# Kernel optimization log

Measured on AMD Instinct MI355X. Metric: run time of the kernel, lower is better.

## Reference

```python
import jax, jax.numpy as jnp
import numpy as np

B, I, J = 2, 2048, 2048
DIM = 1024
H = 16
DH = 64
INNER = H * DH
EPS = 1e-5


def _layernorm(x, g, b):
    mu = jnp.mean(x, axis=-1, keepdims=True)
    var = jnp.var(x, axis=-1, keepdims=True)
    return (x - mu) * jax.lax.rsqrt(var + EPS) * g + b


def setup_inputs() -> dict:
    key = jax.random.key(0)
    ks = jax.random.split(key, 12)
    s_in = 1.0 / np.sqrt(DIM)
    s_inner = 1.0 / np.sqrt(INNER)
    s_h = 1.0 / np.sqrt(H)
    return {
        "x": jax.random.normal(ks[0], (B, I, DIM), jnp.float32),
        "context": jax.random.normal(ks[1], (B, J, DIM), jnp.float32),
        "ln_g": jnp.ones((DIM,), jnp.float32),
        "ln_b": jnp.zeros((DIM,), jnp.float32),
        "ctx_ln_g": jnp.ones((DIM,), jnp.float32),
        "ctx_ln_b": jnp.zeros((DIM,), jnp.float32),
        "W_qk": jax.random.normal(ks[2], (DIM, INNER), jnp.float32) * s_in,
        "W_ctx_qk": jax.random.normal(ks[3], (DIM, INNER), jnp.float32) * s_in,
        "W_v": jax.random.normal(ks[4], (DIM, INNER), jnp.float32) * s_in,
        "W_ctx_v": jax.random.normal(ks[5], (DIM, INNER), jnp.float32) * s_in,
        "W_out": jax.random.normal(ks[6], (INNER, DIM), jnp.float32) * s_inner,
        "b_out": jnp.zeros((DIM,), jnp.float32),
        "W_ctx_out": jax.random.normal(ks[7], (INNER, DIM), jnp.float32) * s_inner,
        "b_ctx_out": jnp.zeros((DIM,), jnp.float32),
        "th_w": jax.random.normal(ks[8], (H, H), jnp.float32) * s_h,
        "ctx_th_w": jax.random.normal(ks[9], (H, H), jnp.float32) * s_h,
    }


def reference(x, context, ln_g, ln_b, ctx_ln_g, ctx_ln_b, W_qk, W_ctx_qk,
              W_v, W_ctx_v, W_out, b_out, W_ctx_out, b_ctx_out, th_w, ctx_th_w):
    b, i, j = x.shape[0], x.shape[1], context.shape[1]
    scale = DH ** -0.5
    xn = _layernorm(x, ln_g, ln_b)
    cn = _layernorm(context, ctx_ln_g, ctx_ln_b)

    def split_heads(t):  # [b, n, h*d] -> [b, h, n, d]
        return t.reshape(t.shape[0], t.shape[1], H, DH).transpose(0, 2, 1, 3)

    qk = split_heads(xn @ W_qk)            # [b, h, i, d]
    ctx_qk = split_heads(cn @ W_ctx_qk)    # [b, h, j, d]
    v = split_heads(xn @ W_v)              # [b, h, i, d]
    ctx_v = split_heads(cn @ W_ctx_v)      # [b, h, j, d]

    sim = jnp.einsum('bhid,bhjd->bhij', qk, ctx_qk) * scale  # shared sim matrix
    attn = jax.nn.softmax(sim, axis=-1)       # softmax over j
    ctx_attn = jax.nn.softmax(sim, axis=-2)   # softmax over i

    # talking heads: 1x1 conv over head dim
    attn = jnp.einsum('gh,bhij->bgij', th_w, attn)
    ctx_attn = jnp.einsum('gh,bhij->bgij', ctx_th_w, ctx_attn)

    out = jnp.einsum('bhij,bhjd->bhid', attn, ctx_v)       # [b, h, i, d]
    ctx_out = jnp.einsum('bhij,bhid->bhjd', ctx_attn, v)   # [b, h, j, d]

    def merge_heads(t):  # [b, h, n, d] -> [b, n, h*d]
        return t.transpose(0, 2, 1, 3).reshape(t.shape[0], t.shape[2], INNER)

    out = merge_heads(out) @ W_out + b_out
    ctx_out = merge_heads(ctx_out) @ W_ctx_out + b_ctx_out
    return out, ctx_out
```

## Files before the change

kernel.cpp:

```cpp
#include <hip/hip_runtime.h>
#include <hip/hip_bf16.h>
#include <cstdint>

#define DIM_   1024
#define H_     16
#define DH_    64
#define INNER_ 1024
#define B_     2
#define I_     2048
#define J_     2048
#define SCALE_ 0.125f

using bf16x8 = __attribute__((ext_vector_type(8))) short;
using f32x4  = __attribute__((ext_vector_type(4))) float;

__device__ __forceinline__ unsigned short f2bf(float f) {
  unsigned int u = __float_as_uint(f);
  u = (u + 0x7FFFu + ((u >> 16) & 1u)) >> 16;
  return (unsigned short)u;
}
__device__ __forceinline__ float bf2f(unsigned short h) {
  return __uint_as_float(((unsigned int)h) << 16);
}

__global__ __launch_bounds__(256) void ln_cast_kernel(
    const float* __restrict__ in, const float* __restrict__ g,
    const float* __restrict__ bb, unsigned short* __restrict__ out) {
  int row = blockIdx.x;
  int t = threadIdx.x;
  const float4* rp = (const float4*)(in + (size_t)row * DIM_);
  float4 v = rp[t];
  float s  = v.x + v.y + v.z + v.w;
  float ss = v.x * v.x + v.y * v.y + v.z * v.z + v.w * v.w;
  for (int o = 1; o < 64; o <<= 1) {
    s  += __shfl_xor(s, o, 64);
    ss += __shfl_xor(ss, o, 64);
  }
  __shared__ float ls[4], lss[4];
  int wave = t >> 6, lane = t & 63;
  if (lane == 0) { ls[wave] = s; lss[wave] = ss; }
  __syncthreads();
  s  = ls[0] + ls[1] + ls[2] + ls[3];
  ss = lss[0] + lss[1] + lss[2] + lss[3];
  float mu  = s * (1.0f / DIM_);
  float var = ss * (1.0f / DIM_) - mu * mu;
  float rstd = rsqrtf(var + 1e-5f);
  float4 gv = ((const float4*)g)[t];
  float4 bv = ((const float4*)bb)[t];
  ushort4 o4;
  o4.x = f2bf((v.x - mu) * rstd * gv.x + bv.x);
  o4.y = f2bf((v.y - mu) * rstd * gv.y + bv.y);
  o4.z = f2bf((v.z - mu) * rstd * gv.z + bv.z);
  o4.w = f2bf((v.w - mu) * rstd * gv.w + bv.w);
  ((ushort4*)(out + (size_t)row * DIM_))[t] = o4;
}

__global__ __launch_bounds__(256) void transpose_cast_f32(
    const float* __restrict__ in, unsigned short* __restrict__ out, int R, int C) {
  __shared__ float tile[32][33];
  int z = blockIdx.z;
  const float* ip = in + (size_t)z * R * C;
  unsigned short* op = out + (size_t)z * R * C;
  int c0 = blockIdx.x * 32, r0 = blockIdx.y * 32;
  int tx = threadIdx.x, ty = threadIdx.y;
  for (int k = 0; k < 4; k++)
    tile[ty * 4 + k][tx] = ip[(size_t)(r0 + ty * 4 + k) * C + c0 + tx];
  __syncthreads();
  for (int k = 0; k < 4; k++)
    op[(size_t)(c0 + ty * 4 + k) * R + r0 + tx] = f2bf(tile[tx][ty * 4 + k]);
}

__global__ __launch_bounds__(256) void transpose_bf16(
    const unsigned short* __restrict__ in, unsigned short* __restrict__ out, int R, int C) {
  __shared__ unsigned short tile[32][33];
  int z = blockIdx.z;
  const unsigned short* ip = in + (size_t)z * R * C;
  unsigned short* op = out + (size_t)z * R * C;
  int c0 = blockIdx.x * 32, r0 = blockIdx.y * 32;
  int tx = threadIdx.x, ty = threadIdx.y;
  for (int k = 0; k < 4; k++)
    tile[ty * 4 + k][tx] = ip[(size_t)(r0 + ty * 4 + k) * C + c0 + tx];
  __syncthreads();
  for (int k = 0; k < 4; k++)
    op[(size_t)(c0 + ty * 4 + k) * R + r0 + tx] = tile[tx][ty * 4 + k];
}

#define LDP 40
__global__ __launch_bounds__(256) void gemm_bt(
    const unsigned short* __restrict__ A, const unsigned short* __restrict__ Bt,
    const float* __restrict__ bias, void* __restrict__ Cout,
    int M, int N, int K, int c_f32) {
  __shared__ unsigned short As[128 * LDP];
  __shared__ unsigned short Bs[128 * LDP];
  int t = threadIdx.x;
  int lane = t & 63, wave = t >> 6;
  int m0 = blockIdx.y * 128, n0 = blockIdx.x * 128;
  int wm = (wave >> 1) * 64, wn = (wave & 1) * 64;
  int l15 = lane & 15, lk = lane >> 4;
  int lrow = t >> 2, lc8 = (t & 3) * 8;
  f32x4 acc[4][4] = {};

  for (int k0 = 0; k0 < K; k0 += 32) {
    *(bf16x8*)&As[lrow * LDP + lc8]        = *(const bf16x8*)&A[(size_t)(m0 + lrow) * K + k0 + lc8];
    *(bf16x8*)&As[(lrow + 64) * LDP + lc8] = *(const bf16x8*)&A[(size_t)(m0 + lrow + 64) * K + k0 + lc8];
    *(bf16x8*)&Bs[lrow * LDP + lc8]        = *(const bf16x8*)&Bt[(size_t)(n0 + lrow) * K + k0 + lc8];
    *(bf16x8*)&Bs[(lrow + 64) * LDP + lc8] = *(const bf16x8*)&Bt[(size_t)(n0 + lrow + 64) * K + k0 + lc8];
    __syncthreads();
    bf16x8 af[4], bfr[4];
#pragma unroll
    for (int mi = 0; mi < 4; mi++) af[mi]  = *(const bf16x8*)&As[(wm + mi * 16 + l15) * LDP + lk * 8];
#pragma unroll
    for (int ni = 0; ni < 4; ni++) bfr[ni] = *(const bf16x8*)&Bs[(wn + ni * 16 + l15) * LDP + lk * 8];
#pragma unroll
    for (int mi = 0; mi < 4; mi++)
#pragma unroll
      for (int ni = 0; ni < 4; ni++)
        acc[mi][ni] = __builtin_amdgcn_mfma_f32_16x16x32_bf16(af[mi], bfr[ni], acc[mi][ni], 0, 0, 0);
    __syncthreads();
  }
#pragma unroll
  for (int mi = 0; mi < 4; mi++)
#pragma unroll
    for (int ni = 0; ni < 4; ni++) {
      int col = n0 + wn + ni * 16 + l15;
      float bsv = bias ? bias[col] : 0.0f;
#pragma unroll
      for (int r = 0; r < 4; r++) {
        int row = m0 + wm + mi * 16 + lk * 4 + r;
        float val = acc[mi][ni][r] + bsv;
        if (c_f32) ((float*)Cout)[(size_t)row * N + col] = val;
        else ((unsigned short*)Cout)[(size_t)row * N + col] = f2bf(val);
      }
    }
}

__global__ __launch_bounds__(256) void stats_kernel(
    const unsigned short* __restrict__ Q, const unsigned short* __restrict__ Kc,
    float* __restrict__ rsum, int NQ, int NK) {
  int b = blockIdx.z, h = blockIdx.y, i0 = blockIdx.x * 32;
  int t = threadIdx.x, lane = t & 63, wave = t >> 6;
  int l15 = lane & 15, lk = lane >> 4;
  const size_t qbase = ((size_t)b * NQ + i0) * INNER_ + h * DH_;
  bf16x8 af[2][2];
#pragma unroll
  for (int mi = 0; mi < 2; mi++)
#pragma unroll
    for (int ks = 0; ks < 2; ks++)
      af[mi][ks] = *(const bf16x8*)&Q[qbase + (size_t)(mi * 16 + l15) * INNER_ + ks * 32 + lk * 8];
  float racc[2][4] = {};
  for (int j0 = wave * 16; j0 < NK; j0 += 64) {
    const size_t kbase = ((size_t)b * NK + j0 + l15) * INNER_ + h * DH_ + lk * 8;
    bf16x8 b0 = *(const bf16x8*)&Kc[kbase];
    bf16x8 b1 = *(const bf16x8*)&Kc[kbase + 32];
#pragma unroll
    for (int mi = 0; mi < 2; mi++) {
      f32x4 acc = {};
      acc = __builtin_amdgcn_mfma_f32_16x16x32_bf16(af[mi][0], b0, acc, 0, 0, 0);
      acc = __builtin_amdgcn_mfma_f32_16x16x32_bf16(af[mi][1], b1, acc, 0, 0, 0);
#pragma unroll
      for (int r = 0; r < 4; r++) racc[mi][r] += __expf(acc[r] * SCALE_);
    }
  }
#pragma unroll
  for (int o = 1; o < 16; o <<= 1)
#pragma unroll
    for (int mi = 0; mi < 2; mi++)
#pragma unroll
      for (int r = 0; r < 4; r++) racc[mi][r] += __shfl_xor(racc[mi][r], o, 64);
  __shared__ float part[4][32];
  if (l15 == 0)
#pragma unroll
    for (int mi = 0; mi < 2; mi++)
#pragma unroll
      for (int r = 0; r < 4; r++) part[wave][mi * 16 + lk * 4 + r] = racc[mi][r];
  __syncthreads();
  if (t < 32)
    rsum[((size_t)b * H_ + h) * NQ + i0 + t] = part[0][t] + part[1][t] + part[2][t] + part[3][t];
}

#define MSROW 40
#define MSG   (32 * MSROW + 8)
__global__ __launch_bounds__(256, 2) void fused_attn_kernel(
    const unsigned short* __restrict__ Q, const unsigned short* __restrict__ Kc,
    const unsigned short* __restrict__ Vt, const float* __restrict__ rsum,
    const float* __restrict__ thw,
    float* __restrict__ p0, float* __restrict__ p1,
    float* __restrict__ p2, float* __restrict__ p3,
    int NQ, int NK, int CHUNK) {
  __shared__ unsigned short Pb[4 * 256 * 16];
  __shared__ unsigned short Ms[16 * MSG];
  __shared__ float rinvS[512];
  int n = blockIdx.x;
  int combo = n & 7;
  int b = combo >> 2, jc = combo & 3;
  int i0 = (n >> 3) * 32;
  float* __restrict__ Op = (jc == 0) ? p0 : (jc == 1) ? p1 : (jc == 2) ? p2 : p3;
  int t = threadIdx.x, lane = t & 63, wave = t >> 6;
  int l15 = lane & 15, lk = lane >> 4;

  rinvS[t]       = 1.0f / rsum[((size_t)b * H_ + (t >> 5)) * NQ + i0 + (t & 31)];
  rinvS[t + 256] = 1.0f / rsum[((size_t)b * H_ + ((t + 256) >> 5)) * NQ + i0 + (t & 31)];

  bf16x8 tfrag;
  {
    int part = lk >> 1, hb = (lk & 1) * 8;
#pragma unroll
    for (int e = 0; e < 8; e++) {
      float a = thw[l15 * H_ + hb + e];
      unsigned short hi = f2bf(a);
      tfrag[e] = (short)(part == 0 ? hi : f2bf(a - bf2f(hi)));
    }
  }
  __syncthreads();

  bf16x8 qpre[4][2][2];
#pragma unroll
  for (int hh = 0; hh < 4; hh++)
#pragma unroll
    for (int is = 0; is < 2; is++)
#pragma unroll
      for (int kk = 0; kk < 2; kk++)
        qpre[hh][is][kk] = *(const bf16x8*)&Q[((size_t)b * NQ + i0 + is * 16 + l15) * INNER_
                                              + (wave * 4 + hh) * 64 + kk * 32 + lk * 8];

  f32x4 acc[32] = {};
  const int jbeg = jc * CHUNK;

  for (int js = 0; js < CHUNK; js += 32) {
    int j0 = jbeg + js;
    const unsigned short* Kb0 = Kc + ((size_t)b * NK + j0 + l15) * INNER_;
    const unsigned short* Kb1 = Kb0 + (size_t)16 * INNER_;
    unsigned int stage[2][2][4][2];
#pragma unroll
    for (int hh = 0; hh < 4; hh++) {
      int h = wave * 4 + hh;
      bf16x8 kb00 = *(const bf16x8*)&Kb0[h * 64 + lk * 8];
      bf16x8 kb01 = *(const bf16x8*)&Kb0[h * 64 + 32 + lk * 8];
      bf16x8 kb10 = *(const bf16x8*)&Kb1[h * 64 + lk * 8];
      bf16x8 kb11 = *(const bf16x8*)&Kb1[h * 64 + 32 + lk * 8];
#pragma unroll
      for (int is = 0; is < 2; is++) {
        f32x4 s0 = {}, s1 = {};
        s0 = __builtin_amdgcn_mfma_f32_16x16x32_bf16(qpre[hh][is][0], kb00, s0, 0, 0, 0);
        s0 = __builtin_amdgcn_mfma_f32_16x16x32_bf16(qpre[hh][is][1], kb01, s0, 0, 0, 0);
        s1 = __builtin_amdgcn_mfma_f32_16x16x32_bf16(qpre[hh][is][0], kb10, s1, 0, 0, 0);
        s1 = __builtin_amdgcn_mfma_f32_16x16x32_bf16(qpre[hh][is][1], kb11, s1, 0, 0, 0);
        f32x4 ri = *(const f32x4*)&rinvS[h * 32 + is * 16 + lk * 4];
#pragma unroll
        for (int r = 0; r < 4; r++) {
          unsigned int b0 = f2bf(__expf(s0[r] * SCALE_) * ri[r]);
          unsigned int b1 = f2bf(__expf(s1[r] * SCALE_) * ri[r]);
          if (hh & 1) { stage[is][0][r][hh >> 1] |= b0 << 16; stage[is][1][r][hh >> 1] |= b1 << 16; }
          else        { stage[is][0][r][hh >> 1]  = b0;       stage[is][1][r][hh >> 1]  = b1; }
        }
      }
    }
#pragma unroll
    for (int is = 0; is < 2; is++)
#pragma unroll
      for (int jp = 0; jp < 2; jp++)
#pragma unroll
        for (int r = 0; r < 4; r++) {
          int row = (lk * 4 + r) * 16 + l15;
          int col = (wave * 4) ^ ((row & 1) << 3);
          uint2 u = { stage[is][jp][r][0], stage[is][jp][r][1] };
          *(uint2*)&Pb[(is + jp * 2) * 256 * 16 + row * 16 + col] = u;
        }
    __syncthreads();
    {
      int isub = wave & 1, jstrip = wave >> 1;
      const unsigned short* pr = &Pb[(isub + jstrip * 2) * 256 * 16];
#pragma unroll
      for (int p = 0; p < 16; p++) {
        int row = p * 16 + l15;
        int col = ((lk & 1) << 3) ^ ((row & 1) << 3);
        bf16x8 af = *(const bf16x8*)&pr[row * 16 + col];
        f32x4 m = {};
        m = __builtin_amdgcn_mfma_f32_16x16x32_bf16(af, tfrag, m, 0, 0, 0);
        ushort4 o;
        o.x = f2bf(m[0]); o.y = f2bf(m[1]); o.z = f2bf(m[2]); o.w = f2bf(m[3]);
        *(ushort4*)&Ms[l15 * MSG + (isub * 16 + p) * MSROW + jstrip * 16 + lk * 4] = o;
      }
    }
    __syncthreads();
#pragma unroll
    for (int gi = 0; gi < 4; gi++) {
      int g = wave * 4 + gi;
      bf16x8 ma0 = *(const bf16x8*)&Ms[g * MSG + l15 * MSROW + lk * 8];
      bf16x8 ma1 = *(const bf16x8*)&Ms[g * MSG + (16 + l15) * MSROW + lk * 8];
#pragma unroll
      for (int nt = 0; nt < 4; nt++) {
        const size_t vb = ((size_t)b * INNER_ + g * 64 + nt * 16 + l15) * NK + j0 + lk * 8;
        bf16x8 v0 = *(const bf16x8*)&Vt[vb];
        acc[gi * 8 + nt]     = __builtin_amdgcn_mfma_f32_16x16x32_bf16(ma0, v0, acc[gi * 8 + nt], 0, 0, 0);
        acc[gi * 8 + 4 + nt] = __builtin_amdgcn_mfma_f32_16x16x32_bf16(ma1, v0, acc[gi * 8 + 4 + nt], 0, 0, 0);
      }
    }
  }
#pragma unroll
  for (int gi = 0; gi < 4; gi++)
#pragma unroll
    for (int is = 0; is < 2; is++)
#pragma unroll
      for (int nt = 0; nt < 4; nt++) {
        int col = (wave * 4 + gi) * 64 + nt * 16 + l15;
#pragma unroll
        for (int r = 0; r < 4; r++)
          Op[((size_t)b * NQ + i0 + is * 16 + lk * 4 + r) * INNER_ + col] = acc[gi * 8 + is * 4 + nt][r];
      }
}

__global__ __launch_bounds__(256) void reduce_cast_kernel(
    const float* __restrict__ p0, const float* __restrict__ p1,
    const float* __restrict__ p2, const float* __restrict__ p3,
    unsigned short* __restrict__ out, int n4) {
  int idx = blockIdx.x * 256 + threadIdx.x;
  if (idx >= n4) return;
  float4 v = ((const float4*)p0)[idx];
  float4 w = ((const float4*)p1)[idx];
  float4 a = ((const float4*)p2)[idx];
  float4 c = ((const float4*)p3)[idx];
  v.x += w.x + a.x + c.x; v.y += w.y + a.y + c.y;
  v.z += w.z + a.z + c.z; v.w += w.w + a.w + c.w;
  ushort4 o;
  o.x = f2bf(v.x); o.y = f2bf(v.y); o.z = f2bf(v.z); o.w = f2bf(v.w);
  ((ushort4*)out)[idx] = o;
}

extern "C" void kernel_launch(void* const* d_in, const int* in_sizes, int n_in,
                              void* d_out, int out_size, void* d_ws, size_t ws_size,
                              hipStream_t stream) {
  const float* x      = (const float*)d_in[0];
  const float* ctx    = (const float*)d_in[1];
  const float* ln_g   = (const float*)d_in[2];
  const float* ln_b   = (const float*)d_in[3];
  const float* cln_g  = (const float*)d_in[4];
  const float* cln_b  = (const float*)d_in[5];
  const float* W_qk   = (const float*)d_in[6];
  const float* W_cqk  = (const float*)d_in[7];
  const float* W_v    = (const float*)d_in[8];
  const float* W_cv   = (const float*)d_in[9];
  const float* W_out  = (const float*)d_in[10];
  const float* b_out  = (const float*)d_in[11];
  const float* W_cout = (const float*)d_in[12];
  const float* b_cout = (const float*)d_in[13];
  const float* th_w   = (const float*)d_in[14];
  const float* cth_w  = (const float*)d_in[15];

  char* w = (char*)d_ws;
  const size_t SZ_ROW = (size_t)B_ * I_ * DIM_ * 2;
  const size_t SZ_W   = (size_t)DIM_ * INNER_ * 2;
  unsigned short* xn    = (unsigned short*)w; w += SZ_ROW;
  unsigned short* cn    = (unsigned short*)w; w += SZ_ROW;
  unsigned short* Wqkt  = (unsigned short*)w; w += SZ_W;
  unsigned short* Wcqkt = (unsigned short*)w; w += SZ_W;
  unsigned short* Wvt   = (unsigned short*)w; w += SZ_W;
  unsigned short* Wcvt  = (unsigned short*)w; w += SZ_W;
  unsigned short* Woutt = (unsigned short*)w; w += SZ_W;
  unsigned short* Wcoutt= (unsigned short*)w; w += SZ_W;
  unsigned short* qk    = (unsigned short*)w; w += SZ_ROW;
  unsigned short* ck    = (unsigned short*)w; w += SZ_ROW;
  unsigned short* vv    = (unsigned short*)w; w += SZ_ROW;
  unsigned short* cv    = (unsigned short*)w; w += SZ_ROW;
  unsigned short* vT    = (unsigned short*)w; w += SZ_ROW;
  unsigned short* cvT   = (unsigned short*)w; w += SZ_ROW;
  float* rsum = (float*)w; w += (size_t)B_ * H_ * I_ * 4;
  float* csum = (float*)w; w += (size_t)B_ * H_ * J_ * 4;
  unsigned short* Oh1 = (unsigned short*)w; w += SZ_ROW;
  unsigned short* Oh2 = (unsigned short*)w; w += SZ_ROW;

  const size_t PART = (size_t)B_ * I_ * INNER_ * 4;
  float* p0 = (float*)xn;
  float* p1 = (float*)vv;
  float* p2 = (float*)w;
  float* p3 = (float*)(w + PART);

  dim3 tb(32, 8);
  ln_cast_kernel<<<B_ * I_, 256, 0, stream>>>(x, ln_g, ln_b, xn);
  ln_cast_kernel<<<B_ * J_, 256, 0, stream>>>(ctx, cln_g, cln_b, cn);

  transpose_cast_f32<<<dim3(32, 32, 1), tb, 0, stream>>>(W_qk,   Wqkt,  DIM_, INNER_);
  transpose_cast_f32<<<dim3(32, 32, 1), tb, 0, stream>>>(W_cqk,  Wcqkt, DIM_, INNER_);
  transpose_cast_f32<<<dim3(32, 32, 1), tb, 0, stream>>>(W_v,    Wvt,   DIM_, INNER_);
  transpose_cast_f32<<<dim3(32, 32, 1), tb, 0, stream>>>(W_cv,   Wcvt,  DIM_, INNER_);
  transpose_cast_f32<<<dim3(32, 32, 1), tb, 0, stream>>>(W_out,  Woutt, INNER_, DIM_);
  transpose_cast_f32<<<dim3(32, 32, 1), tb, 0, stream>>>(W_cout, Wcoutt,INNER_, DIM_);

  gemm_bt<<<dim3(INNER_ / 128, (B_ * I_) / 128), 256, 0, stream>>>(xn, Wqkt,  nullptr, qk, B_ * I_, INNER_, DIM_, 0);
  gemm_bt<<<dim3(INNER_ / 128, (B_ * J_) / 128), 256, 0, stream>>>(cn, Wcqkt, nullptr, ck, B_ * J_, INNER_, DIM_, 0);
  gemm_bt<<<dim3(INNER_ / 128, (B_ * I_) / 128), 256, 0, stream>>>(xn, Wvt,   nullptr, vv, B_ * I_, INNER_, DIM_, 0);
  gemm_bt<<<dim3(INNER_ / 128, (B_ * J_) / 128), 256, 0, stream>>>(cn, Wcvt,  nullptr, cv, B_ * J_, INNER_, DIM_, 0);

  transpose_bf16<<<dim3(INNER_ / 32, I_ / 32, B_), tb, 0, stream>>>(vv, vT, I_, INNER_);
  transpose_bf16<<<dim3(INNER_ / 32, J_ / 32, B_), tb, 0, stream>>>(cv, cvT, J_, INNER_);

  stats_kernel<<<dim3(I_ / 32, H_, B_), 256, 0, stream>>>(qk, ck, rsum, I_, J_);
  stats_kernel<<<dim3(J_ / 32, H_, B_), 256, 0, stream>>>(ck, qk, csum, J_, I_);

  const int n4 = (B_ * I_ * INNER_) / 4;
  fused_attn_kernel<<<(I_ / 32) * 4 * B_, 256, 0, stream>>>(
      qk, ck, cvT, rsum, th_w, p0, p1, p2, p3, I_, J_, J_ / 4);
  reduce_cast_kernel<<<n4 / 256, 256, 0, stream>>>(p0, p1, p2, p3, Oh1, n4);
  fused_attn_kernel<<<(J_ / 32) * 4 * B_, 256, 0, stream>>>(
      ck, qk, vT, csum, cth_w, p0, p1, p2, p3, J_, I_, I_ / 4);
  reduce_cast_kernel<<<n4 / 256, 256, 0, stream>>>(p0, p1, p2, p3, Oh2, n4);

  gemm_bt<<<dim3(DIM_ / 128, (B_ * I_) / 128), 256, 0, stream>>>(Oh1, Woutt, b_out, (float*)d_out, B_ * I_, DIM_, INNER_, 1);
  gemm_bt<<<dim3(DIM_ / 128, (B_ * J_) / 128), 256, 0, stream>>>(Oh2, Wcoutt, b_cout, ((float*)d_out) + (size_t)B_ * I_ * DIM_, B_ * J_, DIM_, INNER_, 1);
}
```

Measured before the change: 924.7 us.

## Batch projection GEMMs and stats launches, raise MFMA wave priority in attention

Concatenates the transposed QK and V weights so one batched GEMM launch (grid z over x/context) produces all four projections, and merges the two output projections into one launch. The stats kernel now handles both softmax directions in one launch and 64 rows per block, so each loaded K fragment is reused across more rows. The fused attention kernel wraps its MFMA sequences in s_setprio to favour issuing matrix ops across waves. The goal is fewer launches and tail effects, more reuse in stats, and better MFMA issue, at the cost of more registers in the stats kernel.

Result: faster. 806.4 us (-12.8%).

```diff
diff --git a/kernel.cpp b/kernel.cpp
--- a/kernel.cpp
+++ b/kernel.cpp
@@ -86,12 +86,19 @@
 }
 
 #define LDP 40
-__global__ __launch_bounds__(256) void gemm_bt(
-    const unsigned short* __restrict__ A, const unsigned short* __restrict__ Bt,
-    const float* __restrict__ bias, void* __restrict__ Cout,
-    int M, int N, int K, int c_f32) {
+__global__ __launch_bounds__(256) void gemm_qkv(
+    const unsigned short* __restrict__ A0, const unsigned short* __restrict__ A1,
+    const unsigned short* __restrict__ Bt0, const unsigned short* __restrict__ Bt1,
+    unsigned short* __restrict__ qkO0, unsigned short* __restrict__ vO0,
+    unsigned short* __restrict__ qkO1, unsigned short* __restrict__ vO1,
+    int M, int K) {
   __shared__ unsigned short As[128 * LDP];
   __shared__ unsigned short Bs[128 * LDP];
+  int z = blockIdx.z;
+  const unsigned short* A  = z ? A1 : A0;
+  const unsigned short* Bt = z ? Bt1 : Bt0;
+  unsigned short* qkO = z ? qkO1 : qkO0;
+  unsigned short* vO  = z ? vO1 : vO0;
   int t = threadIdx.x;
   int lane = t & 63, wave = t >> 6;
   int m0 = blockIdx.y * 128, n0 = blockIdx.x * 128;
@@ -118,42 +125,99 @@
         acc[mi][ni] = __builtin_amdgcn_mfma_f32_16x16x32_bf16(af[mi], bfr[ni], acc[mi][ni], 0, 0, 0);
     __syncthreads();
   }
+  unsigned short* dst = (n0 < 1024) ? qkO : vO;
+  int nbase = n0 & 1023;
+#pragma unroll
+  for (int mi = 0; mi < 4; mi++)
+#pragma unroll
+    for (int ni = 0; ni < 4; ni++) {
+      int col = nbase + wn + ni * 16 + l15;
+#pragma unroll
+      for (int r = 0; r < 4; r++) {
+        int row = m0 + wm + mi * 16 + lk * 4 + r;
+        dst[(size_t)row * INNER_ + col] = f2bf(acc[mi][ni][r]);
+      }
+    }
+}
+
+__global__ __launch_bounds__(256) void gemm_out(
+    const unsigned short* __restrict__ A0, const unsigned short* __restrict__ A1,
+    const unsigned short* __restrict__ Bt0, const unsigned short* __restrict__ Bt1,
+    const float* __restrict__ bias0, const float* __restrict__ bias1,
+    float* __restrict__ C0, float* __restrict__ C1,
+    int M, int N, int K) {
+  __shared__ unsigned short As[128 * LDP];
+  __shared__ unsigned short Bs[128 * LDP];
+  int z = blockIdx.z;
+  const unsigned short* A  = z ? A1 : A0;
+  const unsigned short* Bt = z ? Bt1 : Bt0;
+  const float* bias = z ? bias1 : bias0;
+  float* Cout = z ? C1 : C0;
+  int t = threadIdx.x;
+  int lane = t & 63, wave = t >> 6;
+  int m0 = blockIdx.y * 128, n0 = blockIdx.x * 128;
+  int wm = (wave >> 1) * 64, wn = (wave & 1) * 64;
+  int l15 = lane & 15, lk = lane >> 4;
+  int lrow = t >> 2, lc8 = (t & 3) * 8;
+  f32x4 acc[4][4] = {};
+
+  for (int k0 = 0; k0 < K; k0 += 32) {
+    *(bf16x8*)&As[lrow * LDP + lc8]        = *(const bf16x8*)&A[(size_t)(m0 + lrow) * K + k0 + lc8];
+    *(bf16x8*)&As[(lrow + 64) * LDP + lc8] = *(const bf16x8*)&A[(size_t)(m0 + lrow + 64) * K + k0 + lc8];
+    *(bf16x8*)&Bs[lrow * LDP + lc8]        = *(const bf16x8*)&Bt[(size_t)(n0 + lrow) * K + k0 + lc8];
+    *(bf16x8*)&Bs[(lrow + 64) * LDP + lc8] = *(const bf16x8*)&Bt[(size_t)(n0 + lrow + 64) * K + k0 + lc8];
+    __syncthreads();
+    bf16x8 af[4], bfr[4];
+#pragma unroll
+    for (int mi = 0; mi < 4; mi++) af[mi]  = *(const bf16x8*)&As[(wm + mi * 16 + l15) * LDP + lk * 8];
+#pragma unroll
+    for (int ni = 0; ni < 4; ni++) bfr[ni] = *(const bf16x8*)&Bs[(wn + ni * 16 + l15) * LDP + lk * 8];
+#pragma unroll
+    for (int mi = 0; mi < 4; mi++)
+#pragma unroll
+      for (int ni = 0; ni < 4; ni++)
+        acc[mi][ni] = __builtin_amdgcn_mfma_f32_16x16x32_bf16(af[mi], bfr[ni], acc[mi][ni], 0, 0, 0);
+    __syncthreads();
+  }
 #pragma unroll
   for (int mi = 0; mi < 4; mi++)
 #pragma unroll
     for (int ni = 0; ni < 4; ni++) {
       int col = n0 + wn + ni * 16 + l15;
-      float bsv = bias ? bias[col] : 0.0f;
+      float bsv = bias[col];
 #pragma unroll
       for (int r = 0; r < 4; r++) {
         int row = m0 + wm + mi * 16 + lk * 4 + r;
-        float val = acc[mi][ni][r] + bsv;
-        if (c_f32) ((float*)Cout)[(size_t)row * N + col] = val;
-        else ((unsigned short*)Cout)[(size_t)row * N + col] = f2bf(val);
+        Cout[(size_t)row * N + col] = acc[mi][ni][r] + bsv;
       }
     }
 }
 
 __global__ __launch_bounds__(256) void stats_kernel(
-    const unsigned short* __restrict__ Q, const unsigned short* __restrict__ Kc,
-    float* __restrict__ rsum, int NQ, int NK) {
-  int b = blockIdx.z, h = blockIdx.y, i0 = blockIdx.x * 32;
+    const unsigned short* __restrict__ qk, const unsigned short* __restrict__ ck,
+    float* __restrict__ rsum, float* __restrict__ csum, int NQ, int NK) {
+  int zz = blockIdx.z;
+  int b = zz & 1, dir = zz >> 1;
+  const unsigned short* Q  = dir ? ck : qk;
+  const unsigned short* Kc = dir ? qk : ck;
+  float* out = dir ? csum : rsum;
+  int h = blockIdx.y, i0 = blockIdx.x * 64;
   int t = threadIdx.x, lane = t & 63, wave = t >> 6;
   int l15 = lane & 15, lk = lane >> 4;
   const size_t qbase = ((size_t)b * NQ + i0) * INNER_ + h * DH_;
-  bf16x8 af[2][2];
-#pragma unroll
-  for (int mi = 0; mi < 2; mi++)
+  bf16x8 af[4][2];
+#pragma unroll
+  for (int mi = 0; mi < 4; mi++)
 #pragma unroll
     for (int ks = 0; ks < 2; ks++)
       af[mi][ks] = *(const bf16x8*)&Q[qbase + (size_t)(mi * 16 + l15) * INNER_ + ks * 32 + lk * 8];
-  float racc[2][4] = {};
+  float racc[4][4] = {};
   for (int j0 = wave * 16; j0 < NK; j0 += 64) {
     const size_t kbase = ((size_t)b * NK + j0 + l15) * INNER_ + h * DH_ + lk * 8;
     bf16x8 b0 = *(const bf16x8*)&Kc[kbase];
     bf16x8 b1 = *(const bf16x8*)&Kc[kbase + 32];
 #pragma unroll
-    for (int mi = 0; mi < 2; mi++) {
+    for (int mi = 0; mi < 4; mi++) {
       f32x4 acc = {};
       acc = __builtin_amdgcn_mfma_f32_16x16x32_bf16(af[mi][0], b0, acc, 0, 0, 0);
       acc = __builtin_amdgcn_mfma_f32_16x16x32_bf16(af[mi][1], b1, acc, 0, 0, 0);
@@ -164,18 +228,18 @@
 #pragma unroll
   for (int o = 1; o < 16; o <<= 1)
 #pragma unroll
-    for (int mi = 0; mi < 2; mi++)
+    for (int mi = 0; mi < 4; mi++)
 #pragma unroll
       for (int r = 0; r < 4; r++) racc[mi][r] += __shfl_xor(racc[mi][r], o, 64);
-  __shared__ float part[4][32];
+  __shared__ float part[4][64];
   if (l15 == 0)
 #pragma unroll
-    for (int mi = 0; mi < 2; mi++)
+    for (int mi = 0; mi < 4; mi++)
 #pragma unroll
       for (int r = 0; r < 4; r++) part[wave][mi * 16 + lk * 4 + r] = racc[mi][r];
   __syncthreads();
-  if (t < 32)
-    rsum[((size_t)b * H_ + h) * NQ + i0 + t] = part[0][t] + part[1][t] + part[2][t] + part[3][t];
+  if (t < 64)
+    out[((size_t)b * H_ + h) * NQ + i0 + t] = part[0][t] + part[1][t] + part[2][t] + part[3][t];
 }
 
 #define MSROW 40
@@ -241,10 +305,12 @@
 #pragma unroll
       for (int is = 0; is < 2; is++) {
         f32x4 s0 = {}, s1 = {};
+        __builtin_amdgcn_s_setprio(1);
         s0 = __builtin_amdgcn_mfma_f32_16x16x32_bf16(qpre[hh][is][0], kb00, s0, 0, 0, 0);
         s0 = __builtin_amdgcn_mfma_f32_16x16x32_bf16(qpre[hh][is][1], kb01, s0, 0, 0, 0);
         s1 = __builtin_amdgcn_mfma_f32_16x16x32_bf16(qpre[hh][is][0], kb10, s1, 0, 0, 0);
         s1 = __builtin_amdgcn_mfma_f32_16x16x32_bf16(qpre[hh][is][1], kb11, s1, 0, 0, 0);
+        __builtin_amdgcn_s_setprio(0);
         f32x4 ri = *(const f32x4*)&rinvS[h * 32 + is * 16 + lk * 4];
 #pragma unroll
         for (int r = 0; r < 4; r++) {
@@ -276,7 +342,9 @@
         int col = ((lk & 1) << 3) ^ ((row & 1) << 3);
         bf16x8 af = *(const bf16x8*)&pr[row * 16 + col];
         f32x4 m = {};
+        __builtin_amdgcn_s_setprio(1);
         m = __builtin_amdgcn_mfma_f32_16x16x32_bf16(af, tfrag, m, 0, 0, 0);
+        __builtin_amdgcn_s_setprio(0);
         ushort4 o;
         o.x = f2bf(m[0]); o.y = f2bf(m[1]); o.z = f2bf(m[2]); o.w = f2bf(m[3]);
         *(ushort4*)&Ms[l15 * MSG + (isub * 16 + p) * MSROW + jstrip * 16 + lk * 4] = o;
@@ -292,8 +360,10 @@
       for (int nt = 0; nt < 4; nt++) {
         const size_t vb = ((size_t)b * INNER_ + g * 64 + nt * 16 + l15) * NK + j0 + lk * 8;
         bf16x8 v0 = *(const bf16x8*)&Vt[vb];
+        __builtin_amdgcn_s_setprio(1);
         acc[gi * 8 + nt]     = __builtin_amdgcn_mfma_f32_16x16x32_bf16(ma0, v0, acc[gi * 8 + nt], 0, 0, 0);
         acc[gi * 8 + 4 + nt] = __builtin_amdgcn_mfma_f32_16x16x32_bf16(ma1, v0, acc[gi * 8 + 4 + nt], 0, 0, 0);
+        __builtin_amdgcn_s_setprio(0);
       }
     }
   }
@@ -352,10 +422,8 @@
   const size_t SZ_W   = (size_t)DIM_ * INNER_ * 2;
   unsigned short* xn    = (unsigned short*)w; w += SZ_ROW;
   unsigned short* cn    = (unsigned short*)w; w += SZ_ROW;
-  unsigned short* Wqkt  = (unsigned short*)w; w += SZ_W;
-  unsigned short* Wcqkt = (unsigned short*)w; w += SZ_W;
-  unsigned short* Wvt   = (unsigned short*)w; w += SZ_W;
-  unsigned short* Wcvt  = (unsigned short*)w; w += SZ_W;
+  unsigned short* WqvX  = (unsigned short*)w; w += 2 * SZ_W;
+  unsigned short* WqvC  = (unsigned short*)w; w += 2 * SZ_W;
   unsigned short* Woutt = (unsigned short*)w; w += SZ_W;
   unsigned short* Wcoutt= (unsigned short*)w; w += SZ_W;
   unsigned short* qk    = (unsigned short*)w; w += SZ_ROW;
@@ -379,23 +447,21 @@
   ln_cast_kernel<<<B_ * I_, 256, 0, stream>>>(x, ln_g, ln_b, xn);
   ln_cast_kernel<<<B_ * J_, 256, 0, stream>>>(ctx, cln_g, cln_b, cn);
 
-  transpose_cast_f32<<<dim3(32, 32, 1), tb, 0, stream>>>(W_qk,   Wqkt,  DIM_, INNER_);
-  transpose_cast_f32<<<dim3(32, 32, 1), tb, 0, stream>>>(W_cqk,  Wcqkt, DIM_, INNER_);
-  transpose_cast_f32<<<dim3(32, 32, 1), tb, 0, stream>>>(W_v,    Wvt,   DIM_, INNER_);
-  transpose_cast_f32<<<dim3(32, 32, 1), tb, 0, stream>>>(W_cv,   Wcvt,  DIM_, INNER_);
+  const size_t WOFF = (size_t)DIM_ * INNER_;
+  transpose_cast_f32<<<dim3(32, 32, 1), tb, 0, stream>>>(W_qk,   WqvX,        DIM_, INNER_);
+  transpose_cast_f32<<<dim3(32, 32, 1), tb, 0, stream>>>(W_v,    WqvX + WOFF, DIM_, INNER_);
+  transpose_cast_f32<<<dim3(32, 32, 1), tb, 0, stream>>>(W_cqk,  WqvC,        DIM_, INNER_);
+  transpose_cast_f32<<<dim3(32, 32, 1), tb, 0, stream>>>(W_cv,   WqvC + WOFF, DIM_, INNER_);
   transpose_cast_f32<<<dim3(32, 32, 1), tb, 0, stream>>>(W_out,  Woutt, INNER_, DIM_);
   transpose_cast_f32<<<dim3(32, 32, 1), tb, 0, stream>>>(W_cout, Wcoutt,INNER_, DIM_);
 
-  gemm_bt<<<dim3(INNER_ / 128, (B_ * I_) / 128), 256, 0, stream>>>(xn, Wqkt,  nullptr, qk, B_ * I_, INNER_, DIM_, 0);
-  gemm_bt<<<dim3(INNER_ / 128, (B_ * J_) / 128), 256, 0, stream>>>(cn, Wcqkt, nullptr, ck, B_ * J_, INNER_, DIM_, 0);
-  gemm_bt<<<dim3(INNER_ / 128, (B_ * I_) / 128), 256, 0, stream>>>(xn, Wvt,   nullptr, vv, B_ * I_, INNER_, DIM_, 0);
-  gemm_bt<<<dim3(INNER_ / 128, (B_ * J_) / 128), 256, 0, stream>>>(cn, Wcvt,  nullptr, cv, B_ * J_, INNER_, DIM_, 0);
+  gemm_qkv<<<dim3(2 * INNER_ / 128, (B_ * I_) / 128, 2), 256, 0, stream>>>(
+      xn, cn, WqvX, WqvC, qk, vv, ck, cv, B_ * I_, DIM_);
 
   transpose_bf16<<<dim3(INNER_ / 32, I_ / 32, B_), tb, 0, stream>>>(vv, vT, I_, INNER_);
   transpose_bf16<<<dim3(INNER_ / 32, J_ / 32, B_), tb, 0, stream>>>(cv, cvT, J_, INNER_);
 
-  stats_kernel<<<dim3(I_ / 32, H_, B_), 256, 0, stream>>>(qk, ck, rsum, I_, J_);
-  stats_kernel<<<dim3(J_ / 32, H_, B_), 256, 0, stream>>>(ck, qk, csum, J_, I_);
+  stats_kernel<<<dim3(I_ / 64, H_, 4), 256, 0, stream>>>(qk, ck, rsum, csum, I_, J_);
 
   const int n4 = (B_ * I_ * INNER_) / 4;
   fused_attn_kernel<<<(I_ / 32) * 4 * B_, 256, 0, stream>>>(
@@ -405,6 +471,8 @@
       ck, qk, vT, csum, cth_w, p0, p1, p2, p3, J_, I_, I_ / 4);
   reduce_cast_kernel<<<n4 / 256, 256, 0, stream>>>(p0, p1, p2, p3, Oh2, n4);
 
-  gemm_bt<<<dim3(DIM_ / 128, (B_ * I_) / 128), 256, 0, stream>>>(Oh1, Woutt, b_out, (float*)d_out, B_ * I_, DIM_, INNER_, 1);
-  gemm_bt<<<dim3(DIM_ / 128, (B_ * J_) / 128), 256, 0, stream>>>(Oh2, Wcoutt, b_cout, ((float*)d_out) + (size_t)B_ * I_ * DIM_, B_ * J_, DIM_, INNER_, 1);
-}
+  gemm_out<<<dim3(DIM_ / 128, (B_ * I_) / 128, 2), 256, 0, stream>>>(
+      Oh1, Oh2, Woutt, Wcoutt, b_out, b_cout,
+      (float*)d_out, ((float*)d_out) + (size_t)B_ * I_ * DIM_,
+      B_ * I_, DIM_, INNER_);
+}
```
